# Kernel optimization log

Measured on AMD Instinct MI355X. Metric: run time of the kernel, lower is better.

Reference implementation:

```python
import jax, jax.numpy as jnp
import numpy as np

OFFS = [[0, -1], [-1, 0], [-1, -1], [0, -2], [-2, 0], [-2, -2], [0, -3], [-3, 0], [-3, -3]]
SIGMA = 1.2  # module's self.sigma; overseg_factor == 1.0 so the aff scaling is a no-op


def _gauss_kernel(sigma, truncate=4.0):
    # matches scipy/skimage gaussian: radius = int(truncate*sigma + 0.5)
    r = int(truncate * sigma + 0.5)
    t = np.arange(-r, r + 1)
    k = np.exp(-0.5 * (t / sigma) ** 2)
    return jnp.asarray(k / k.sum(), jnp.float32), r


def _blur_axis(x, k, r, axis):
    # x: [C,H,W]; skimage default mode='nearest' -> edge padding
    pad = [(0, 0)] * x.ndim
    pad[axis] = (r, r)
    xp = jnp.pad(x, pad, mode='edge')
    n = x.shape[axis]
    out = k[0] * jax.lax.slice_in_dim(xp, 0, n, axis=axis)
    for i in range(1, 2 * r + 1):
        out = out + k[i] * jax.lax.slice_in_dim(xp, i, i + n, axis=axis)
    return out


def gaussian_blur(x, sigma):
    k, r = _gauss_kernel(sigma)
    return _blur_axis(_blur_axis(x, k, r, 1), k, r, 2)


def naive_affinities(raw, offs):
    # per-offset intensity-difference affinity, normalized by its max
    affs = []
    for off in offs:
        rolled = jnp.roll(raw, (-off[0], -off[1]), axis=(-2, -1))
        d = jnp.sqrt(((raw - rolled) ** 2).sum(0))  # norm over channel dim
        affs.append(d / d.max())
    return jnp.stack(affs)  # [9,H,W]


def setup_inputs() -> dict:
    key = jax.random.key(0)
    k1, k2, k3, k4 = jax.random.split(key, 4)
    B, E, H, W = 4, 32, 512, 512
    return {
        'embeds': jax.random.normal(k1, (B, E, H, W), jnp.float32),
        'tf_embeds': jax.random.normal(k2, (B, E, H, W), jnp.float32),
        'raw': jax.random.uniform(k3, (1, 1, H, W), jnp.float32),
        'mask': jax.random.uniform(k4, (1, 9, H, W), jnp.float32),
    }


def reference(embeds, tf_embeds, raw, mask):
    r = raw[0]      # [C,H,W]
    m = mask[0]     # [9,H,W]
    affs = naive_affinities(gaussian_blur(r, SIGMA), OFFS)
    # sep_chnl scaling with overseg_factor=1.0 is identity; clamp as in torch
    affs = jnp.clip(affs, 0.0, 1.0)
    loss = jnp.zeros((), embeds.dtype)
    for i, off in enumerate(OFFS):
        rolled = jnp.roll(tf_embeds, (-off[0], -off[1]), axis=(-2, -1))
        dist = (1.0 - (embeds * rolled).sum(1)) * m[i][None]  # [B,H,W]
        a = affs[i] - affs[i].min()
        a = a / a.max()
        loss = loss + (dist * (0.5 - a)[None]).mean()
    return loss
```

## Files before the change

### kernel.cpp

```cpp
#include <hip/hip_runtime.h>
#include <math.h>

#define Hh 512
#define Ww 512
#define Bb 4
#define Ee 32
#define PLANE (Hh*Ww)
#define NOFF 9

#define WS_BLUR   0
#define WS_MIN    524304
#define WS_MAX    524320
#define WS_ACC    524336
#define WS_CNT    524338

__device__ __constant__ int d_OH[NOFF] = {0,-1,-1,0,-2,-2,0,-3,-3};
__device__ __constant__ int d_OW[NOFF] = {-1,0,-1,-2,0,-2,-3,0,-3};

#define TS 32
#define HALO 5
__global__ __launch_bounds__(256) void k_blur(const float* __restrict__ raw,
                                              float* __restrict__ ws){
    __shared__ float sraw[TS+2*HALO][TS+2*HALO+1];
    __shared__ float shb [TS][TS+2*HALO+1];
    int tx = blockIdx.x & 15, ty = blockIdx.x >> 4;
    int r0 = ty*TS - HALO, c0 = tx*TS - HALO;

    double kd[11], s = 0.0;
    #pragma unroll
    for (int i = 0; i < 11; i++){
        double x = (double)(i - 5) / 1.2;
        kd[i] = exp(-0.5 * x * x);
        s += kd[i];
    }
    float w[11];
    #pragma unroll
    for (int i = 0; i < 11; i++) w[i] = (float)(kd[i] / s);

    for (int t = threadIdx.x; t < 42*42; t += 256){
        int rr = t / 42, cc = t - rr*42;
        int gr = min(max(r0+rr, 0), Hh-1);
        int gc = min(max(c0+cc, 0), Ww-1);
        sraw[rr][cc] = raw[gr*Ww + gc];
    }
    __syncthreads();
    for (int t = threadIdx.x; t < TS*42; t += 256){
        int rr = t / 42, cc = t - rr*42;
        float a = 0.f;
        #pragma unroll
        for (int i = 0; i < 11; i++) a += w[i] * sraw[rr+i][cc];
        shb[rr][cc] = a;
    }
    __syncthreads();
    for (int t = threadIdx.x; t < TS*TS; t += 256){
        int rr = t >> 5, cc = t & 31;
        float a = 0.f;
        #pragma unroll
        for (int i = 0; i < 11; i++) a += w[i] * shb[rr][cc+i];
        ws[WS_BLUR + (ty*TS+rr)*Ww + (tx*TS+cc)] = a;
    }
    if (blockIdx.x == 0){
        if (threadIdx.x < 16){
            ((unsigned int*)(ws + WS_MIN))[threadIdx.x] = 0x7F800000u;
            ((unsigned int*)(ws + WS_MAX))[threadIdx.x] = 0u;
        }
        if (threadIdx.x == 0){
            *(double*)(ws + WS_ACC) = 0.0;
            *(unsigned int*)(ws + WS_CNT) = 0u;
        }
    }
}

__global__ void k_minmax(float* __restrict__ ws){
    int idx = blockIdx.x * 512 + threadIdx.x;
    int h = idx >> 9, w = idx & 511;
    float bc = ws[WS_BLUR + idx];
    int lane = threadIdx.x & 63, wv = threadIdx.x >> 6;
    __shared__ float smn[8 * NOFF], smx[8 * NOFF];
    #pragma unroll
    for (int i = 0; i < NOFF; i++){
        int hn = (h + d_OH[i]) & (Hh-1);
        int wn = (w + d_OW[i]) & (Ww-1);
        float d = fabsf(bc - ws[WS_BLUR + hn * Ww + wn]);
        float mnv = d, mxv = d;
        for (int s = 32; s; s >>= 1){
            mnv = fminf(mnv, __shfl_xor(mnv, s));
            mxv = fmaxf(mxv, __shfl_xor(mxv, s));
        }
        if (lane == 0){ smn[wv * NOFF + i] = mnv; smx[wv * NOFF + i] = mxv; }
    }
    __syncthreads();
    if (threadIdx.x < NOFF){
        float mnv = smn[threadIdx.x], mxv = smx[threadIdx.x];
        for (int v = 1; v < 8; v++){
            mnv = fminf(mnv, smn[v * NOFF + threadIdx.x]);
            mxv = fmaxf(mxv, smx[v * NOFF + threadIdx.x]);
        }
        atomicMin((unsigned int*)(ws + WS_MIN) + threadIdx.x, __float_as_uint(mnv));
        atomicMax((unsigned int*)(ws + WS_MAX) + threadIdx.x, __float_as_uint(mxv));
    }
}

struct TT { float4 l0,o0,l1,o1,l2,o2,l3,o3, ev; };

__global__ __launch_bounds__(512)
void k_main(const float* __restrict__ E, const float* __restrict__ T,
            const float* __restrict__ mask, float* __restrict__ ws,
            float* __restrict__ out){
    int blk = blockIdx.x;
    int bb  = blk >> 7;
    int row4 = (blk & 127) << 2;
    int rq  = threadIdx.x >> 7;
    int wq  = threadIdx.x & 127;
    int hr  = row4 + rq;
    int c0  = wq << 2;
    int cl  = (c0 - 4) & 511;
    int rr1 = (hr-1)&511, rr2 = (hr-2)&511, rr3 = (hr-3)&511;
    int pix = hr * Ww + c0;

    int ro0 = pix,         lo0 = hr*Ww + cl;
    int ro1 = rr1*Ww + c0, lo1 = rr1*Ww + cl;
    int ro2 = rr2*Ww + c0, lo2 = rr2*Ww + cl;
    int ro3 = rr3*Ww + c0, lo3 = rr3*Ww + cl;

    const float* bl = ws + WS_BLUR;
    float tb[4][8];
    {
        float4 v;
        v = *(const float4*)(bl + lo0); tb[0][0]=v.x; tb[0][1]=v.y; tb[0][2]=v.z; tb[0][3]=v.w;
        v = *(const float4*)(bl + ro0); tb[0][4]=v.x; tb[0][5]=v.y; tb[0][6]=v.z; tb[0][7]=v.w;
        v = *(const float4*)(bl + lo1); tb[1][0]=v.x; tb[1][1]=v.y; tb[1][2]=v.z; tb[1][3]=v.w;
        v = *(const float4*)(bl + ro1); tb[1][4]=v.x; tb[1][5]=v.y; tb[1][6]=v.z; tb[1][7]=v.w;
        v = *(const float4*)(bl + lo2); tb[2][0]=v.x; tb[2][1]=v.y; tb[2][2]=v.z; tb[2][3]=v.w;
        v = *(const float4*)(bl + ro2); tb[2][4]=v.x; tb[2][5]=v.y; tb[2][6]=v.z; tb[2][7]=v.w;
        v = *(const float4*)(bl + lo3); tb[3][0]=v.x; tb[3][1]=v.y; tb[3][2]=v.z; tb[3][3]=v.w;
        v = *(const float4*)(bl + ro3); tb[3][4]=v.x; tb[3][5]=v.y; tb[3][6]=v.z; tb[3][7]=v.w;
    }
    const unsigned int* mnb = (const unsigned int*)(ws + WS_MIN);
    const unsigned int* mxb = (const unsigned int*)(ws + WS_MAX);
    float mn[NOFF], inv[NOFF];
    #pragma unroll
    for (int i = 0; i < NOFF; i++){
        mn[i]  = __uint_as_float(mnb[i]);
        inv[i] = 1.f / (__uint_as_float(mxb[i]) - mn[i]);
    }
    float c[4][NOFF];
    float acc[4];
    #pragma unroll
    for (int j = 0; j < 4; j++){
        float bc = tb[0][4+j];
        float d[NOFF];
        d[0] = fabsf(bc - tb[0][3+j]);
        d[1] = fabsf(bc - tb[1][4+j]);
        d[2] = fabsf(bc - tb[1][3+j]);
        d[3] = fabsf(bc - tb[0][2+j]);
        d[4] = fabsf(bc - tb[2][4+j]);
        d[5] = fabsf(bc - tb[2][2+j]);
        d[6] = fabsf(bc - tb[0][1+j]);
        d[7] = fabsf(bc - tb[3][4+j]);
        d[8] = fabsf(bc - tb[3][1+j]);
        acc[j] = 0.f;
        #pragma unroll
        for (int i = 0; i < NOFF; i++){
            float a = (d[i] - mn[i]) * inv[i];
            float mv = ((const float*)(mask + i * PLANE + pix))[j];
            c[j][i] = mv * (0.5f - a);
            acc[j] += c[j][i];
        }
    }

    const float* Tb = T + (size_t)bb * Ee * PLANE;
    const float* Eb = E + (size_t)bb * Ee * PLANE + pix;

    auto LD = [&](TT& d, int e){
        const float* Tp = Tb + (size_t)e * PLANE;
        d.l0 = *(const float4*)(Tp + lo0); d.o0 = *(const float4*)(Tp + ro0);
        d.l1 = *(const float4*)(Tp + lo1); d.o1 = *(const float4*)(Tp + ro1);
        d.l2 = *(const float4*)(Tp + lo2); d.o2 = *(const float4*)(Tp + ro2);
        d.l3 = *(const float4*)(Tp + lo3); d.o3 = *(const float4*)(Tp + ro3);
        d.ev = *(const float4*)(Eb + (size_t)e * PLANE);
    };
    auto CMP = [&](const TT& t){
        float t0[8] = {t.l0.x,t.l0.y,t.l0.z,t.l0.w, t.o0.x,t.o0.y,t.o0.z,t.o0.w};
        float t1[8] = {t.l1.x,t.l1.y,t.l1.z,t.l1.w, t.o1.x,t.o1.y,t.o1.z,t.o1.w};
        float t2[8] = {t.l2.x,t.l2.y,t.l2.z,t.l2.w, t.o2.x,t.o2.y,t.o2.z,t.o2.w};
        float t3[8] = {t.l3.x,t.l3.y,t.l3.z,t.l3.w, t.o3.x,t.o3.y,t.o3.z,t.o3.w};
        float ev[4] = {t.ev.x, t.ev.y, t.ev.z, t.ev.w};
        #pragma unroll
        for (int j = 0; j < 4; j++){
            float s =        c[j][0] * t0[3+j];
            s = fmaf(c[j][1], t1[4+j], s);
            s = fmaf(c[j][2], t1[3+j], s);
            s = fmaf(c[j][3], t0[2+j], s);
            s = fmaf(c[j][4], t2[4+j], s);
            s = fmaf(c[j][5], t2[2+j], s);
            s = fmaf(c[j][6], t0[1+j], s);
            s = fmaf(c[j][7], t3[4+j], s);
            s = fmaf(c[j][8], t3[1+j], s);
            acc[j] = fmaf(-ev[j], s, acc[j]);
        }
    };

    TT ta, tc;
    LD(ta, 0);
    #pragma unroll 1
    for (int e = 0; e < Ee-2; e += 2){
        LD(tc, e+1);
        CMP(ta);
        LD(ta, e+2);
        CMP(tc);
    }
    LD(tc, Ee-1);
    CMP(ta);
    CMP(tc);

    float part = acc[0] + acc[1] + acc[2] + acc[3];

    for (int s = 32; s; s >>= 1) part += __shfl_xor(part, s);
    __shared__ float sp[8];
    int lane = threadIdx.x & 63, wv = threadIdx.x >> 6;
    if (lane == 0) sp[wv] = part;
    __syncthreads();
    if (threadIdx.x == 0){
        float bs = 0.f;
        #pragma unroll
        for (int v = 0; v < 8; v++) bs += sp[v];
        double* accp = (double*)(ws + WS_ACC);
        atomicAdd(accp, (double)bs);
        __threadfence();
        unsigned int done = atomicAdd((unsigned int*)(ws + WS_CNT), 1u);
        if (done == gridDim.x - 1){
            double v = atomicAdd(accp, 0.0);
            out[0] = (float)(v / (double)((size_t)Bb * PLANE));
        }
    }
}

extern "C" void kernel_launch(void* const* d_in, const int* in_sizes, int n_in,
                              void* d_out, int out_size, void* d_ws, size_t ws_size,
                              hipStream_t stream) {
    const float* embeds = (const float*)d_in[0];
    const float* tf     = (const float*)d_in[1];
    const float* raw    = (const float*)d_in[2];
    const float* mask   = (const float*)d_in[3];
    float* ws  = (float*)d_ws;
    float* out = (float*)d_out;

    k_blur  <<<256, 256, 0, stream>>>(raw, ws);
    k_minmax<<<PLANE/512, 512, 0, stream>>>(ws);
    k_main  <<<512, 512, 0, stream>>>(embeds, tf, mask, ws, out);
}
```

Measured before the change: 105.7 us.

## Split embedding channel loop across blocks to raise grid parallelism

The main kernel grid grows from 512 to 2048 blocks. Each block now handles one of four 8-channel slices of the 32 embedding channels instead of all 32. Only the first slice adds the constant mask term to the accumulator. This gives more blocks to fill the GPU's compute units and more memory parallelism. In exchange, each block recomputes the blur-difference coefficients and rereads the mask, and there are four times as many double atomic adds and counter increments.

After: 156.0 us. +47.5%, slower.

```diff
diff --git a/kernel.cpp b/kernel.cpp
--- a/kernel.cpp
+++ b/kernel.cpp
@@ -7,6 +7,7 @@
 #define Ee 32
 #define PLANE (Hh*Ww)
 #define NOFF 9
+#define EC 8
 
 #define WS_BLUR   0
 #define WS_MIN    524304
@@ -108,10 +109,17 @@
             const float* __restrict__ mask, float* __restrict__ ws,
             float* __restrict__ out){
     int blk = blockIdx.x;
-    int bb  = blk >> 7;
-    int row4 = (blk & 127) << 2;
-    int rq  = threadIdx.x >> 7;
-    int wq  = threadIdx.x & 127;
+    int bb  = blk >> 9;
+    int ec  = (blk >> 7) & 3;
+    int rg  = blk & 127;
+    int row4 = rg << 2;
+    int e0  = ec * EC;
+
+    int tid = threadIdx.x;
+    int rq  = tid >> 7;
+    int wq  = tid & 127;
+    int wv  = tid >> 6;
+    int ln  = tid & 63;
     int hr  = row4 + rq;
     int c0  = wq << 2;
     int cl  = (c0 - 4) & 511;
@@ -146,6 +154,7 @@
     }
     float c[4][NOFF];
     float acc[4];
+    float csw = (ec == 0) ? 1.f : 0.f;
     #pragma unroll
     for (int j = 0; j < 4; j++){
         float bc = tb[0][4+j];
@@ -165,7 +174,7 @@
             float a = (d[i] - mn[i]) * inv[i];
             float mv = ((const float*)(mask + i * PLANE + pix))[j];
             c[j][i] = mv * (0.5f - a);
-            acc[j] += c[j][i];
+            acc[j] = fmaf(csw, c[j][i], acc[j]);
         }
     }
 
@@ -202,26 +211,24 @@
     };
 
     TT ta, tc;
-    LD(ta, 0);
+    LD(ta, e0);
     #pragma unroll 1
-    for (int e = 0; e < Ee-2; e += 2){
-        LD(tc, e+1);
+    for (int ei = 0; ei < EC-2; ei += 2){
+        LD(tc, e0+ei+1);
         CMP(ta);
-        LD(ta, e+2);
+        LD(ta, e0+ei+2);
         CMP(tc);
     }
-    LD(tc, Ee-1);
+    LD(tc, e0+EC-1);
     CMP(ta);
     CMP(tc);
 
     float part = acc[0] + acc[1] + acc[2] + acc[3];
-
     for (int s = 32; s; s >>= 1) part += __shfl_xor(part, s);
     __shared__ float sp[8];
-    int lane = threadIdx.x & 63, wv = threadIdx.x >> 6;
-    if (lane == 0) sp[wv] = part;
-    __syncthreads();
-    if (threadIdx.x == 0){
+    if (ln == 0) sp[wv] = part;
+    __syncthreads();
+    if (tid == 0){
         float bs = 0.f;
         #pragma unroll
         for (int v = 0; v < 8; v++) bs += sp[v];
@@ -248,5 +255,5 @@
 
     k_blur  <<<256, 256, 0, stream>>>(raw, ws);
     k_minmax<<<PLANE/512, 512, 0, stream>>>(ws);
-    k_main  <<<512, 512, 0, stream>>>(embeds, tf, mask, ws, out);
-}
+    k_main  <<<2048, 512, 0, stream>>>(embeds, tf, mask, ws, out);
+}
```
